# Kernel tuning notes

Measured on AMD Instinct MI355X. Metric: run time of the kernel, lower is better.

Reference implementation:

```python
import jax, jax.numpy as jnp
import numpy as np

IN_DIM = 1024
HID = 1024
DEPTH = 13            # perfect binary tree: 2**13 = 8192 leaves, 8191 internal nodes
N_LEAVES = 2 ** DEPTH
N_TOKENS = 8192
N_OPS = 4             # '+', '/', '*', '-' (ordered_op=False)


def setup_inputs() -> dict:
    key = jax.random.key(0)
    ks = jax.random.split(key, 16)
    sW = 1.0 / np.sqrt(IN_DIM)
    sU = 1.0 / np.sqrt(HID)
    inp = {
        "tokens": jax.random.normal(ks[0], (N_TOKENS, IN_DIM), jnp.float32),
        "leaf_token_ids": jax.random.randint(ks[1], (N_LEAVES,), 0, N_TOKENS),
        "op_ids": jax.random.randint(ks[2], (N_LEAVES - 1,), 0, N_OPS),
        "W_i": jax.random.normal(ks[3], (HID, IN_DIM), jnp.float32) * sW,
        "W_o": jax.random.normal(ks[4], (HID, IN_DIM), jnp.float32) * sW,
        "W_u": jax.random.normal(ks[5], (HID, IN_DIM), jnp.float32) * sW,
        "W_f": jax.random.normal(ks[6], (HID, IN_DIM), jnp.float32) * sW,
        "U_i": jax.random.normal(ks[7], (HID, HID), jnp.float32) * sU,
        "U_o": jax.random.normal(ks[8], (HID, HID), jnp.float32) * sU,
        "U_u": jax.random.normal(ks[9], (HID, HID), jnp.float32) * sU,
        "U_f": jax.random.normal(ks[10], (HID, HID), jnp.float32) * sU,
        "b_i": jnp.zeros((1, HID), jnp.float32),
        "b_o": jnp.zeros((1, HID), jnp.float32),
        "b_u": jnp.zeros((1, HID), jnp.float32),
        "b_f": jnp.zeros((1, HID), jnp.float32),
        "op_emb": jax.random.uniform(ks[11], (N_OPS, IN_DIM), jnp.float32, -1.0, 1.0),
        "c_init": jnp.zeros((2, HID), jnp.float32),
        "h_init": jnp.zeros((2, HID), jnp.float32),
    }
    return inp


def reference(tokens, leaf_token_ids, op_ids, W_i, W_o, W_u, W_f,
              U_i, U_o, U_u, U_f, b_i, b_o, b_u, b_f,
              op_emb, c_init, h_init):
    """Depth-batched Child-Sum TreeLSTM over a perfect binary tree.
    op_ids are stored root-first level order: level l (root=0) occupies
    op_ids[2**l - 1 : 2**(l+1) - 1]. Leaves are level DEPTH.
    Children of node j at level l are nodes 2j, 2j+1 at level l+1.
    Returns jnp.stack([c_root, h_root])  -> [2, 1, HID]."""
    H = U_i.shape[0]

    def node_step(x, c_state, h_state):
        # x: [n, in_dim]; c_state/h_state: [n, 2, H]
        h_sum = h_state.sum(axis=1)                                   # [n, H]
        i = jax.nn.sigmoid(x @ W_i.T + h_sum @ U_i.T + b_i)
        o = jax.nn.sigmoid(x @ W_o.T + h_sum @ U_o.T + b_o)
        u = jnp.tanh(x @ W_u.T + h_sum @ U_u.T + b_u)
        f = jax.nn.sigmoid((x @ W_f.T)[:, None, :] + h_state @ U_f.T + b_f)  # [n,2,H]
        c = i * u + (f * c_state).sum(axis=1)                         # [n, H]
        h = o * jnp.tanh(c)
        return c, h

    n = leaf_token_ids.shape[0]
    depth = int(np.log2(n))
    # leaves: learnable init states, x = embedding of the token
    x = tokens[leaf_token_ids]                                        # [n, in_dim]
    c, h = node_step(x,
                     jnp.broadcast_to(c_init, (n, 2, H)),
                     jnp.broadcast_to(h_init, (n, 2, H)))
    # internal levels, bottom-up
    for l in range(depth - 1, -1, -1):
        m = 2 ** l
        off = m - 1
        x = op_emb[op_ids[off:off + m]]                               # [m, in_dim]
        c, h = node_step(x, c.reshape(m, 2, H), h.reshape(m, 2, H))
    return jnp.stack([c, h])  # [2, 1, H]: root (c, h)
```

## Files before the change

### kernel.cpp

```cpp
#include <hip/hip_runtime.h>

typedef unsigned short u16;
typedef __attribute__((ext_vector_type(4))) unsigned short us4;
typedef __attribute__((ext_vector_type(4))) float f4;
typedef __attribute__((ext_vector_type(8))) short bf16x8;
typedef __attribute__((ext_vector_type(4))) float f32x4;

__device__ __forceinline__ u16 f2bf(float x) {
  unsigned u = __float_as_uint(x);
  return (u16)((u + 0x7FFFu + ((u >> 16) & 1u)) >> 16);
}
__device__ __forceinline__ float b2f(u16 s) {
  return __uint_as_float(((unsigned)s) << 16);
}
__device__ __forceinline__ float sigm(float x) { return 1.f / (1.f + __expf(-x)); }
__device__ __forceinline__ float tanhf_(float x) { return 2.f / (1.f + __expf(-2.f * x)) - 1.f; }

__global__ void setup_kernel(
    const float* __restrict__ tokens, const int* __restrict__ leaf_ids,
    const float* __restrict__ w0, const float* __restrict__ w1,
    const float* __restrict__ w2, const float* __restrict__ w3,
    const float* __restrict__ u0, const float* __restrict__ u1,
    const float* __restrict__ u2, const float* __restrict__ u3,
    const float* __restrict__ b0, const float* __restrict__ b1,
    const float* __restrict__ b2, const float* __restrict__ b3,
    const float* __restrict__ op_emb, const float* __restrict__ h_init,
    u16* __restrict__ Wb, u16* __restrict__ Ub, u16* __restrict__ Xl,
    float* __restrict__ xw, float* __restrict__ leafC) {
  const int bid = blockIdx.x;
  if (bid < 8192) {
    int mat = bid >> 10;
    int off4 = (int)(bid & 1023) * 256 + threadIdx.x;
    const float* src; u16* dst;
    switch (mat) {
      case 0: src = w0; dst = Wb; break;
      case 1: src = w1; dst = Wb + 1048576; break;
      case 2: src = w2; dst = Wb + 2097152; break;
      case 3: src = w3; dst = Wb + 3145728; break;
      case 4: src = u0; dst = Ub; break;
      case 5: src = u1; dst = Ub + 1048576; break;
      case 6: src = u2; dst = Ub + 2097152; break;
      default: src = u3; dst = Ub + 3145728; break;
    }
    f4 v = ((const f4*)src)[off4];
    us4 o = {f2bf(v[0]), f2bf(v[1]), f2bf(v[2]), f2bf(v[3])};
    ((us4*)dst)[off4] = o;
  } else if (bid < 16384) {
    int n = bid - 8192, t = threadIdx.x;
    int tok = leaf_ids[n];
    f4 v = ((const f4*)(tokens + (size_t)tok * 1024))[t];
    us4 o = {f2bf(v[0]), f2bf(v[1]), f2bf(v[2]), f2bf(v[3])};
    ((us4*)(Xl + (size_t)n * 1024))[t] = o;
  } else {
    int id = (bid - 16384) * 256 + threadIdx.x;
    if (id < 16384) {
      int op = id >> 12, g = (id >> 10) & 3, j = id & 1023;
      const float* wsrc; const float* bs;
      switch (g) {
        case 0: wsrc = w0; bs = b0; break;
        case 1: wsrc = w1; bs = b1; break;
        case 2: wsrc = w2; bs = b2; break;
        default: wsrc = w3; bs = b3; break;
      }
      const f4* xr = (const f4*)(op_emb + (size_t)op * 1024);
      const f4* wr = (const f4*)(wsrc + (size_t)j * 1024);
      float s = bs[j];
      for (int k = 0; k < 256; ++k) {
        f4 a = xr[k], b = wr[k];
        s += a[0] * b[0] + a[1] * b[1] + a[2] * b[2] + a[3] * b[3];
      }
      xw[id] = s;
    } else if (id < 21504) {
      int id2 = id - 16384;
      int sel = id2 >> 10, j = id2 & 1023;
      const f4* h0 = (const f4*)h_init;
      const f4* h1 = (const f4*)(h_init + 1024);
      float s;
      if (sel < 3) {
        const float* usrc; const float* bs;
        switch (sel) {
          case 0: usrc = u0; bs = b0; break;
          case 1: usrc = u1; bs = b1; break;
          default: usrc = u2; bs = b2; break;
        }
        const f4* wr = (const f4*)(usrc + (size_t)j * 1024);
        s = bs[j];
        for (int k = 0; k < 256; ++k) {
          f4 a0 = h0[k], a1 = h1[k], b = wr[k];
          s += (a0[0] + a1[0]) * b[0] + (a0[1] + a1[1]) * b[1] +
               (a0[2] + a1[2]) * b[2] + (a0[3] + a1[3]) * b[3];
        }
      } else {
        const f4* hs = (sel == 3) ? h0 : h1;
        const f4* wr = (const f4*)(u3 + (size_t)j * 1024);
        s = b3[j];
        for (int k = 0; k < 256; ++k) {
          f4 a = hs[k], b = wr[k];
          s += a[0] * b[0] + a[1] * b[1] + a[2] * b[2] + a[3] * b[3];
        }
      }
      leafC[id2] = s;
    }
  }
}

template <int NRT, int NCT>
__global__ __launch_bounds__(256, (NRT == 8 ? 2 : 3)) void tree_gemm(
    const u16* __restrict__ A, const u16* __restrict__ Wm,
    const float* __restrict__ consts,
    const int* __restrict__ ops,
    const float* __restrict__ c_in,
    float* __restrict__ c_out, u16* __restrict__ h_out,
    int nrows, int m_parents, int is_leaf, float* __restrict__ out_root) {
  constexpr int ROWS = NRT * 16;
  constexpr int COLS = NCT * 16;
  constexpr int S = 64 / NCT;
  constexpr int LOG2S = (NCT == 2 ? 5 : 4);
  constexpr int NST = NRT / 2;
  constexpr int DBUF = NRT * 2048;
  constexpr int PASSES = (NRT == 8 ? 4 : (NRT == 4 ? 2 : 1));
  constexpr int RPP = ROWS / PASSES;
  constexpr int FPP = RPP / 16;
  constexpr int SMEM_U16 =
      (4 * RPP * 68 > NRT * 2048 ? 4 * RPP * 68 : NRT * 2048);
  __shared__ __align__(16) u16 smem[SMEM_U16];
  char* smem_c = (char*)smem;

  const int tid = threadIdx.x;
  const int wave = tid >> 6;
  const int lane = tid & 63;
  const int stripe = blockIdx.x & (S - 1);
  const int rowblk = blockIdx.x >> LOG2S;
  const int r0 = rowblk * ROWS;
  const int j0 = stripe * COLS;
  const int ln15 = lane & 15, quad = lane >> 4;
  const int sub = lane >> 3, gsel = lane & 7;

  const char* pAsrc[NST];
  unsigned a_dst[NST];
#pragma unroll
  for (int i = 0; i < NST; ++i) {
    int slot = (wave * NST + i) * 8 + sub;
    int row = r0 + slot; if (row >= nrows) row = nrows - 1;
    pAsrc[i] = (const char*)(A + (size_t)row * 1024 + (unsigned)((gsel ^ sub) * 8));
    a_dst[i] = (unsigned)((wave * NST + i) * 1024 + lane * 16);
  }
  const char* pB[NCT];
#pragma unroll
  for (int f = 0; f < NCT; ++f)
    pB[f] = (const char*)(Wm + (size_t)(wave * 1024 + j0 + f * 16 + ln15) * 1024 + quad * 8);

  unsigned a_base[2];
#pragma unroll
  for (int ks = 0; ks < 2; ++ks)
    a_base[ks] = (unsigned)(ln15 * 128 + (((ks * 4 + quad) ^ (ln15 & 7)) * 16));

  f32x4 acc[NRT][NCT];
#pragma unroll
  for (int t = 0; t < NRT; ++t)
#pragma unroll
    for (int f = 0; f < NCT; ++f) acc[t][f] = (f32x4){0.f, 0.f, 0.f, 0.f};

#pragma unroll
  for (int i = 0; i < NST; ++i)
    __builtin_amdgcn_global_load_lds(
        (const __attribute__((address_space(1))) void*)(pAsrc[i]),
        (__attribute__((address_space(3))) void*)(smem_c + a_dst[i]), 16, 0, 0);
  bf16x8 bcur[2][NCT], bnxt[2][NCT];
#pragma unroll
  for (int ks = 0; ks < 2; ++ks)
#pragma unroll
    for (int f = 0; f < NCT; ++f)
      bcur[ks][f] = *(const bf16x8*)(pB[f] + ks * 64);

#pragma unroll
  for (int ch = 0; ch < 16; ++ch) {
    __syncthreads();
    if (ch < 15) {
#pragma unroll
      for (int i = 0; i < NST; ++i)
        __builtin_amdgcn_global_load_lds(
            (const __attribute__((address_space(1))) void*)(pAsrc[i] + (ch + 1) * 128),
            (__attribute__((address_space(3))) void*)(smem_c + ((ch + 1) & 1) * DBUF + a_dst[i]),
            16, 0, 0);
    }
    const unsigned cb = (unsigned)((ch & 1) * DBUF);
    {
      bf16x8 af[NRT];
#pragma unroll
      for (int t = 0; t < NRT; ++t)
        af[t] = *(const bf16x8*)(smem_c + cb + a_base[0] + t * 2048);
#pragma unroll
      for (int t = 0; t < NRT; ++t)
#pragma unroll
        for (int f = 0; f < NCT; ++f)
          acc[t][f] = __builtin_amdgcn_mfma_f32_16x16x32_bf16(af[t], bcur[0][f],
                                                              acc[t][f], 0, 0, 0);
    }
    if (ch < 15) {
#pragma unroll
      for (int ks = 0; ks < 2; ++ks)
#pragma unroll
        for (int f = 0; f < NCT; ++f)
          bnxt[ks][f] = *(const bf16x8*)(pB[f] + (ch + 1) * 128 + ks * 64);
    }
    {
      bf16x8 af[NRT];
#pragma unroll
      for (int t = 0; t < NRT; ++t)
        af[t] = *(const bf16x8*)(smem_c + cb + a_base[1] + t * 2048);
#pragma unroll
      for (int t = 0; t < NRT; ++t)
#pragma unroll
        for (int f = 0; f < NCT; ++f)
          acc[t][f] = __builtin_amdgcn_mfma_f32_16x16x32_bf16(af[t], bcur[1][f],
                                                              acc[t][f], 0, 0, 0);
    }
#pragma unroll
    for (int ks = 0; ks < 2; ++ks)
#pragma unroll
      for (int f = 0; f < NCT; ++f) bcur[ks][f] = bnxt[ks][f];
  }

#pragma unroll
  for (int pass = 0; pass < PASSES; ++pass) {
    __syncthreads();
#pragma unroll
    for (int tt = 0; tt < FPP; ++tt) {
      int t = pass * FPP + tt;
#pragma unroll
      for (int f = 0; f < NCT; ++f)
#pragma unroll
        for (int k = 0; k < 4; ++k) {
          int row = tt * 16 + quad * 4 + k;
          int col = f * 16 + ln15;
          smem[(wave * RPP + row) * 68 + col] = f2bf(acc[t][f][k]);
        }
    }
    __syncthreads();
    const int rbase = r0 + pass * RPP;

    if (is_leaf) {
      for (int e = tid; e < RPP * COLS; e += 256) {
        int r = e / COLS, j = e % COLS;
        int col = j0 + j, n = rbase + r;
        float p0 = b2f(smem[(0 * RPP + r) * 68 + j]);
        float p1 = b2f(smem[(1 * RPP + r) * 68 + j]);
        float p2 = b2f(smem[(2 * RPP + r) * 68 + j]);
        float p3 = b2f(smem[(3 * RPP + r) * 68 + j]);
        float i_ = sigm(p0 + consts[col]);
        float o_ = sigm(p1 + consts[1024 + col]);
        float u_ = tanhf_(p2 + consts[2048 + col]);
        float f0 = sigm(p3 + consts[3072 + col]);
        float f1 = sigm(p3 + consts[4096 + col]);
        float c = i_ * u_ + f0 * c_in[col] + f1 * c_in[1024 + col];
        float h = o_ * tanhf_(c);
        c_out[(size_t)n * 1024 + col] = c;
        h_out[(size_t)n * 1024 + col] = f2bf(h);
      }
    } else {
      for (int e = tid; e < (RPP / 2) * COLS; e += 256) {
        int p = e / COLS, j = e % COLS;
        int np = (rbase >> 1) + p;
        if (np >= m_parents) break;
        int col = j0 + j;
        int op = ops[np];
        const float* xwop = consts + ((unsigned)(op * 4) << 10);
        float p0a = b2f(smem[(0 * RPP + 2 * p) * 68 + j]), p0b = b2f(smem[(0 * RPP + 2 * p + 1) * 68 + j]);
        float p1a = b2f(smem[(1 * RPP + 2 * p) * 68 + j]), p1b = b2f(smem[(1 * RPP + 2 * p + 1) * 68 + j]);
        float p2a = b2f(smem[(2 * RPP + 2 * p) * 68 + j]), p2b = b2f(smem[(2 * RPP + 2 * p + 1) * 68 + j]);
        float p3a = b2f(smem[(3 * RPP + 2 * p) * 68 + j]), p3b = b2f(smem[(3 * RPP + 2 * p + 1) * 68 + j]);
        float i_ = sigm(p0a + p0b + xwop[col]);
        float o_ = sigm(p1a + p1b + xwop[1024 + col]);
        float u_ = tanhf_(p2a + p2b + xwop[2048 + col]);
        float f0 = sigm(p3a + xwop[3072 + col]);
        float f1 = sigm(p3b + xwop[3072 + col]);
        float c = i_ * u_ + f0 * c_in[(size_t)(rbase + 2 * p) * 1024 + col]
                          + f1 * c_in[(size_t)(rbase + 2 * p + 1) * 1024 + col];
        float h = o_ * tanhf_(c);
        if (m_parents == 1) {
          out_root[col] = c;
          out_root[1024 + col] = h;
        } else {
          c_out[(size_t)np * 1024 + col] = c;
          h_out[(size_t)np * 1024 + col] = f2bf(h);
        }
      }
    }
  }
}

extern "C" void kernel_launch(void* const* d_in, const int* in_sizes, int n_in,
                              void* d_out, int out_size, void* d_ws, size_t ws_size,
                              hipStream_t stream) {
  const float* tokens = (const float*)d_in[0];
  const int* leaf_ids = (const int*)d_in[1];
  const int* op_ids = (const int*)d_in[2];
  const float* W0 = (const float*)d_in[3];
  const float* W1 = (const float*)d_in[4];
  const float* W2 = (const float*)d_in[5];
  const float* W3 = (const float*)d_in[6];
  const float* U0 = (const float*)d_in[7];
  const float* U1 = (const float*)d_in[8];
  const float* U2 = (const float*)d_in[9];
  const float* U3 = (const float*)d_in[10];
  const float* B0 = (const float*)d_in[11];
  const float* B1 = (const float*)d_in[12];
  const float* B2 = (const float*)d_in[13];
  const float* B3 = (const float*)d_in[14];
  const float* op_emb = (const float*)d_in[15];
  const float* c_init = (const float*)d_in[16];
  const float* h_init = (const float*)d_in[17];
  float* out = (float*)d_out;

  char* ws = (char*)d_ws;
  u16* Wb = (u16*)ws;
  u16* Ub = Wb + (size_t)4 * 1024 * 1024;
  u16* Xl = Ub + (size_t)4 * 1024 * 1024;
  u16* hA = Xl + (size_t)8192 * 1024;
  u16* hB = hA + (size_t)8192 * 1024;
  float* cA = (float*)(hB + (size_t)4096 * 1024);
  float* cB = cA + (size_t)8192 * 1024;
  float* xw = cB + (size_t)4096 * 1024;
  float* lc = xw + 16 * 1024;

  setup_kernel<<<16468, 256, 0, stream>>>(tokens, leaf_ids,
                                          W0, W1, W2, W3, U0, U1, U2, U3,
                                          B0, B1, B2, B3, op_emb, h_init,
                                          Wb, Ub, Xl, xw, lc);

  tree_gemm<8, 2><<<64 * 32, 256, 0, stream>>>(Xl, Wb, lc, nullptr, c_init,
                                               cA, hA, 8192, 0, 1, out);

  const u16* hin = hA; const float* cin = cA;
  u16* hout = hB; float* cout = cB;
  for (int l = 12; l >= 0; --l) {
    int m = 1 << l;
    int nrows = 2 * m;
    if (nrows >= 2048) {
      tree_gemm<8, 2><<<(nrows / 128) * 32, 256, 0, stream>>>(
          hin, Ub, xw, op_ids + (m - 1), cin, cout, hout, nrows, m, 0, out);
    } else if (nrows >= 1024) {
      tree_gemm<4, 2><<<(nrows / 64) * 32, 256, 0, stream>>>(
          hin, Ub, xw, op_ids + (m - 1), cin, cout, hout, nrows, m, 0, out);
    } else {
      int rg = nrows / 32; if (rg < 1) rg = 1;
      tree_gemm<2, 2><<<rg * 32, 256, 0, stream>>>(
          hin, Ub, xw, op_ids + (m - 1), cin, cout, hout, nrows, m, 0, out);
    }
    const u16* th = hin; hin = hout; hout = (u16*)th;
    const float* tc = cin; cin = cout; cout = (float*)tc;
  }
}
```

Before: 670.2 us.

## Use one wave per dot product in setup and halve epilogue passes in tree GEMM

The setup kernel's constant precomputation (op-embedding times W and init-h times U dot products) now gives each output a full 64-lane wave with coalesced strided loads and a shuffle reduction. Before, one thread looped serially over 1024 elements. The grid grows to cover one wave per output. Separately, the tree GEMM epilogue pass count is reduced (8-row-tile variant from 4 to 2 passes, 4-row-tile from 2 to 1), so fewer shared-memory staging rounds are needed at the cost of a larger shared buffer and possibly lower occupancy.

```diff
diff --git a/kernel.cpp b/kernel.cpp
--- a/kernel.cpp
+++ b/kernel.cpp
@@ -52,9 +52,16 @@
     us4 o = {f2bf(v[0]), f2bf(v[1]), f2bf(v[2]), f2bf(v[3])};
     ((us4*)(Xl + (size_t)n * 1024))[t] = o;
   } else {
-    int id = (bid - 16384) * 256 + threadIdx.x;
-    if (id < 16384) {
-      int op = id >> 12, g = (id >> 10) & 3, j = id & 1023;
+    const int wave = threadIdx.x >> 6, lane = threadIdx.x & 63;
+    const int wid = (bid - 16384) * 4 + wave;
+    const f4* xr;
+    const f4* wr;
+    float bias;
+    bool dual = false;
+    const f4* xr2 = nullptr;
+    float* dst;
+    if (wid < 16384) {
+      int op = wid >> 12, g = (wid >> 10) & 3, j = wid & 1023;
       const float* wsrc; const float* bs;
       switch (g) {
         case 0: wsrc = w0; bs = b0; break;
@@ -62,20 +69,15 @@
         case 2: wsrc = w2; bs = b2; break;
         default: wsrc = w3; bs = b3; break;
       }
-      const f4* xr = (const f4*)(op_emb + (size_t)op * 1024);
-      const f4* wr = (const f4*)(wsrc + (size_t)j * 1024);
-      float s = bs[j];
-      for (int k = 0; k < 256; ++k) {
-        f4 a = xr[k], b = wr[k];
-        s += a[0] * b[0] + a[1] * b[1] + a[2] * b[2] + a[3] * b[3];
-      }
-      xw[id] = s;
-    } else if (id < 21504) {
-      int id2 = id - 16384;
+      xr = (const f4*)(op_emb + (size_t)op * 1024);
+      wr = (const f4*)(wsrc + (size_t)j * 1024);
+      bias = bs[j];
+      dst = xw + wid;
+    } else {
+      int id2 = wid - 16384;
       int sel = id2 >> 10, j = id2 & 1023;
       const f4* h0 = (const f4*)h_init;
       const f4* h1 = (const f4*)(h_init + 1024);
-      float s;
       if (sel < 3) {
         const float* usrc; const float* bs;
         switch (sel) {
@@ -83,24 +85,31 @@
           case 1: usrc = u1; bs = b1; break;
           default: usrc = u2; bs = b2; break;
         }
-        const f4* wr = (const f4*)(usrc + (size_t)j * 1024);
-        s = bs[j];
-        for (int k = 0; k < 256; ++k) {
-          f4 a0 = h0[k], a1 = h1[k], b = wr[k];
-          s += (a0[0] + a1[0]) * b[0] + (a0[1] + a1[1]) * b[1] +
-               (a0[2] + a1[2]) * b[2] + (a0[3] + a1[3]) * b[3];
-        }
+        xr = h0; xr2 = h1; dual = true;
+        wr = (const f4*)(usrc + (size_t)j * 1024);
+        bias = bs[j];
       } else {
-        const f4* hs = (sel == 3) ? h0 : h1;
-        const f4* wr = (const f4*)(u3 + (size_t)j * 1024);
-        s = b3[j];
-        for (int k = 0; k < 256; ++k) {
-          f4 a = hs[k], b = wr[k];
-          s += a[0] * b[0] + a[1] * b[1] + a[2] * b[2] + a[3] * b[3];
-        }
-      }
-      leafC[id2] = s;
-    }
+        xr = (sel == 3) ? h0 : h1;
+        wr = (const f4*)(u3 + (size_t)j * 1024);
+        bias = b3[j];
+      }
+      dst = leafC + id2;
+    }
+    float s = 0.f;
+#pragma unroll
+    for (int i = 0; i < 4; ++i) {
+      int k = lane + 64 * i;
+      f4 a = xr[k];
+      if (dual) {
+        f4 a2 = xr2[k];
+        a[0] += a2[0]; a[1] += a2[1]; a[2] += a2[2]; a[3] += a2[3];
+      }
+      f4 b = wr[k];
+      s += a[0] * b[0] + a[1] * b[1] + a[2] * b[2] + a[3] * b[3];
+    }
+#pragma unroll
+    for (int off = 32; off > 0; off >>= 1) s += __shfl_xor(s, off);
+    if (lane == 0) *dst = s + bias;
   }
 }
 
@@ -118,7 +127,7 @@
   constexpr int LOG2S = (NCT == 2 ? 5 : 4);
   constexpr int NST = NRT / 2;
   constexpr int DBUF = NRT * 2048;
-  constexpr int PASSES = (NRT == 8 ? 4 : (NRT == 4 ? 2 : 1));
+  constexpr int PASSES = (NRT == 8 ? 2 : 1);
   constexpr int RPP = ROWS / PASSES;
   constexpr int FPP = RPP / 16;
   constexpr int SMEM_U16 =
@@ -324,7 +333,7 @@
   float* xw = cB + (size_t)4096 * 1024;
   float* lc = xw + 16 * 1024;
 
-  setup_kernel<<<16468, 256, 0, stream>>>(tokens, leaf_ids,
+  setup_kernel<<<21760, 256, 0, stream>>>(tokens, leaf_ids,
                                           W0, W1, W2, W3, U0, U1, U2, U3,
                                           B0, B1, B2, B3, op_emb, h_init,
                                           Wb, Ub, Xl, xw, lc);
```

Measured after the change: 565.9 us. 15.5% less time.
